# Performance work log

Measured on AMD Instinct MI355X. Metric: run time of the kernel, lower is better.

## Reference

```python
import jax, jax.numpy as jnp
import numpy as np

EPS = 1e-5

def _bn(x, g, b, axes):
    # BatchNorm (training-mode batch statistics), channel axis = 1
    m = jnp.mean(x, axis=axes, keepdims=True)
    v = jnp.var(x, axis=axes, keepdims=True)
    sh = [1] * x.ndim
    sh[1] = -1
    return (x - m) * jax.lax.rsqrt(v + EPS) * g.reshape(sh) + b.reshape(sh)

def _gelu(x):
    return jax.nn.gelu(x, approximate=False)  # torch nn.GELU default (erf)

def _knn_idx(x, k):
    # x: (B, C, N). Negative squared pairwise distance, take k nearest.
    inner = jnp.einsum('bcn,bcm->bnm', x, x)
    sq = jnp.sum(x * x, axis=1)                       # (B, N)
    negd = 2.0 * inner - sq[:, :, None] - sq[:, None, :]
    _, idx = jax.lax.top_k(negd, k)                   # (B, N, k) int32
    return idx

def _graph_feature(x, k):
    # x: (B, C, N) -> (B, 2C, N, k): concat(neighbor - center, center)
    idx = _knn_idx(x, k)
    xt = jnp.transpose(x, (0, 2, 1))                  # (B, N, C)
    nbr = jax.vmap(lambda xb, ib: xb[ib])(xt, idx)    # (B, N, k, C) gather
    ctr = jnp.broadcast_to(xt[:, :, None, :], nbr.shape)
    f = jnp.concatenate([nbr - ctr, ctr], axis=-1)    # (B, N, k, 2C)
    return jnp.transpose(f, (0, 3, 1, 2))             # (B, 2C, N, k)

def _edge_block(x, W, g, b, k):
    # gather -> 1x1 conv -> BN -> GELU -> max over neighbors
    f = _graph_feature(x, k)
    h = jnp.einsum('oi,bink->bonk', W, f)
    h = _gelu(_bn(h, g, b, (0, 2, 3)))
    return jnp.max(h, axis=-1)                        # (B, O, N)


def setup_inputs() -> dict:
    key = jax.random.key(0)
    ks = jax.random.split(key, 16)
    B, C, N, k = 8, 3, 1024, 20
    c = 64
    def w(kk, o, i):
        return jax.random.normal(kk, (o, i), jnp.float32) * (1.0 / np.sqrt(i))
    inp = {
        'x': jax.random.normal(ks[0], (B, C, N), jnp.float32),
        'k': k,
        'W1': w(ks[1], c, 2 * C),            # (64, 6)
        'g1': jnp.ones((c,)), 'b1': jnp.zeros((c,)),
        'W2': w(ks[2], 2 * c, 2 * c),        # (128, 128)
        'g2': jnp.ones((2 * c,)), 'b2': jnp.zeros((2 * c,)),
        'W3': w(ks[3], 4 * c, 4 * c),        # (256, 256)
        'g3': jnp.ones((4 * c,)), 'b3': jnp.zeros((4 * c,)),
        'W4': w(ks[4], 8 * c, 8 * c),        # (512, 512)
        'g4': jnp.ones((8 * c,)), 'b4': jnp.zeros((8 * c,)),
        'W5': w(ks[5], 16 * c, 15 * c),      # (1024, 960) cat(64+128+256+512)
        'g5': jnp.ones((16 * c,)), 'b5': jnp.zeros((16 * c,)),
        'Wl1': w(ks[6], 8 * c, 32 * c),      # (512, 2048), bias=False
        'g6': jnp.ones((8 * c,)), 'b6': jnp.zeros((8 * c,)),
        'Wl2': w(ks[7], 256, 512), 'bl2': jnp.zeros((256,)),
        'g7': jnp.ones((256,)), 'b7': jnp.zeros((256,)),
        'Wl3': w(ks[8], 40, 256), 'bl3': jnp.zeros((40,)),
    }
    return inp


def reference(x, k, W1, g1, b1, W2, g2, b2, W3, g3, b3, W4, g4, b4,
              W5, g5, b5, Wl1, g6, b6, Wl2, bl2, g7, b7, Wl3, bl3):
    x1 = _edge_block(x,  W1, g1, b1, k)   # (B, 64,  N)
    x2 = _edge_block(x1, W2, g2, b2, k)   # (B, 128, N)
    x3 = _edge_block(x2, W3, g3, b3, k)   # (B, 256, N)
    x4 = _edge_block(x3, W4, g4, b4, k)   # (B, 512, N)
    xc = jnp.concatenate([x1, x2, x3, x4], axis=1)  # (B, 960, N)
    h = jnp.einsum('oi,bin->bon', W5, xc)           # (B, 1024, N)
    h = _gelu(_bn(h, g5, b5, (0, 2)))
    mx = jnp.max(h, axis=-1)
    av = jnp.mean(h, axis=-1)
    z = jnp.concatenate([mx, av], axis=1)           # (B, 2048)
    z = z @ Wl1.T                                   # (B, 512), no bias
    z = jax.nn.leaky_relu(_bn(z, g6, b6, (0,)), 0.2)
    z = z @ Wl2.T + bl2                             # (B, 256)
    z = jax.nn.leaky_relu(_bn(z, g7, b7, (0,)), 0.2)
    out = z @ Wl3.T + bl3                           # (B, 40)
    return out
```

## Files before the change

kernel.cpp:

```cpp
#include <hip/hip_runtime.h>
#include <math.h>

#define BB 8
#define NN 1024
#define KNN 20

typedef unsigned short u16;
typedef __bf16 bf16x8 __attribute__((ext_vector_type(8)));
typedef float floatx4 __attribute__((ext_vector_type(4)));

__device__ __forceinline__ float gelu_erf(float x) {
    return 0.5f * x * (1.0f + erff(x * 0.70710678118654752440f));
}

__device__ __forceinline__ u16 f2bf(float f) {
    unsigned int u = __float_as_uint(f);
    unsigned int r = (u + 0x7fffu + ((u >> 16) & 1u)) >> 16;
    return (u16)r;
}
__device__ __forceinline__ float bf2f(u16 h) {
    return __uint_as_float(((unsigned int)h) << 16);
}

#define STATS_BLK 32768
#define STATS_TOTAL (4 * STATS_BLK + 16384)
#define ZERO_TOTAL (STATS_TOTAL + 3 * 8192)

__global__ void k_transpose(const float* __restrict__ x, float* __restrict__ x0,
                            float* __restrict__ sz) {
    int t = blockIdx.x * 256 + threadIdx.x;
    for (int i = t; i < ZERO_TOTAL; i += BB * NN) sz[i] = 0.f;
    if (t >= BB * NN) return;
    int b = t / NN, n = t % NN;
    #pragma unroll
    for (int c = 0; c < 3; ++c) x0[(size_t)t * 3 + c] = x[((size_t)b * 3 + c) * NN + n];
}

#define SEG2 16384
#define SEG3 81920
#define SEG4 344064
#define SEGT 1327104
__global__ void k_prep_w(const float* __restrict__ W2, const float* __restrict__ W3,
                         const float* __restrict__ W4, const float* __restrict__ W5,
                         u16* __restrict__ wh, u16* __restrict__ wl) {
    int t = blockIdx.x * 256 + threadIdx.x;
    if (t >= SEGT) return;
    float v;
    if (t < SEG2) {
        int row = t >> 6, c = t & 63;
        v = (row < 128) ? W2[row * 128 + c]
                        : W2[(row - 128) * 128 + 64 + c] - W2[(row - 128) * 128 + c];
    } else if (t < SEG3) {
        int i = t - SEG2;
        int row = i >> 7, c = i & 127;
        v = (row < 256) ? W3[row * 256 + c]
                        : W3[(row - 256) * 256 + 128 + c] - W3[(row - 256) * 256 + c];
    } else if (t < SEG4) {
        int i = t - SEG3;
        int row = i >> 8, c = i & 255;
        v = (row < 512) ? W4[row * 512 + c]
                        : W4[(row - 512) * 512 + 256 + c] - W4[(row - 512) * 512 + c];
    } else {
        int i = t - SEG4;
        int row = i / 960, c = i % 960;
        v = W5[row * 960 + c];
    }
    u16 h = f2bf(v);
    wh[t] = h;
    wl[t] = f2bf(v - bf2f(h));
}

__global__ void k_negd(const float* __restrict__ X, int SA, int Kc, float* __restrict__ out) {
    int bz = blockIdx.z;
    const float* Xb = X + (size_t)bz * NN * SA;
    float* Cout = out + (size_t)bz * NN * NN;
    int m0 = blockIdx.y * 128, n0 = blockIdx.x * 128;
    __shared__ float As[16][132];
    __shared__ float Bs[16][132];
    __shared__ float sqA[128];
    __shared__ float sqB[128];
    int t = threadIdx.x;
    int tx = t & 15, ty = t >> 4;
    int r = t >> 1, kb = (t & 1) * 8;
    float acc[2][2][4][4] = {};
    float sqa = 0.f, sqb = 0.f;
    for (int k0 = 0; k0 < Kc; k0 += 16) {
        const float* srcA = Xb + (size_t)(m0 + r) * SA + k0 + kb;
        const float* srcB = Xb + (size_t)(n0 + r) * SA + k0 + kb;
        #pragma unroll
        for (int i = 0; i < 8; ++i) {
            float va = (k0 + kb + i < Kc) ? srcA[i] : 0.f;
            float vb = (k0 + kb + i < Kc) ? srcB[i] : 0.f;
            As[kb + i][r] = va;
            Bs[kb + i][r] = vb;
            sqa = fmaf(va, va, sqa);
            sqb = fmaf(vb, vb, sqb);
        }
        __syncthreads();
        #pragma unroll
        for (int kk = 0; kk < 16; ++kk) {
            float4 a0 = *(const float4*)&As[kk][ty * 4];
            float4 a1 = *(const float4*)&As[kk][64 + ty * 4];
            float4 b0 = *(const float4*)&Bs[kk][tx * 4];
            float4 b1 = *(const float4*)&Bs[kk][64 + tx * 4];
            float av[2][4] = {{a0.x, a0.y, a0.z, a0.w}, {a1.x, a1.y, a1.z, a1.w}};
            float bv[2][4] = {{b0.x, b0.y, b0.z, b0.w}, {b1.x, b1.y, b1.z, b1.w}};
            #pragma unroll
            for (int hm = 0; hm < 2; ++hm)
                #pragma unroll
                for (int hn = 0; hn < 2; ++hn)
                    #pragma unroll
                    for (int i = 0; i < 4; ++i)
                        #pragma unroll
                        for (int j = 0; j < 4; ++j)
                            acc[hm][hn][i][j] = fmaf(av[hm][i], bv[hn][j], acc[hm][hn][i][j]);
        }
        __syncthreads();
    }
    sqa += __shfl_xor(sqa, 1);
    sqb += __shfl_xor(sqb, 1);
    if ((t & 1) == 0) { sqA[r] = sqa; sqB[r] = sqb; }
    __syncthreads();
    #pragma unroll
    for (int hm = 0; hm < 2; ++hm)
        #pragma unroll
        for (int i = 0; i < 4; ++i) {
            int lrow = hm * 64 + ty * 4 + i;
            float sm = sqA[lrow];
            float* crow = Cout + (size_t)(m0 + lrow) * NN + n0;
            #pragma unroll
            for (int hn = 0; hn < 2; ++hn) {
                float4 sn = *(const float4*)&sqB[hn * 64 + tx * 4];
                float4 v;
                v.x = 2.f * acc[hm][hn][i][0] - sm - sn.x;
                v.y = 2.f * acc[hm][hn][i][1] - sm - sn.y;
                v.z = 2.f * acc[hm][hn][i][2] - sm - sn.z;
                v.w = 2.f * acc[hm][hn][i][3] - sm - sn.w;
                *(float4*)&crow[hn * 64 + tx * 4] = v;
            }
        }
}

__global__ __launch_bounds__(256) void k_mfma_comb(
    const u16* __restrict__ Ah, const u16* __restrict__ Al,
    const u16* __restrict__ Wh, const u16* __restrict__ Wl,
    const float* __restrict__ sqg,
    float* __restrict__ negdOut, float* __restrict__ uwOut,
    int K, int ldUw) {
    const int lda = 960;
    int bx = blockIdx.x, by = blockIdx.y;
    bool gram = (by < 8);
    int m0, n0, rowBase;
    const u16 *pBh, *pBl;
    size_t ldb;
    float* pC;
    if (gram) {
        int b = bx & 7;
        n0 = (bx >> 3) * 128;
        m0 = by * 128;
        rowBase = b * NN;
        pBh = Ah; pBl = Al; ldb = lda;
        pC = negdOut + (size_t)b * NN * NN;
    } else {
        m0 = bx * 128;
        n0 = (by - 8) * 128;
        rowBase = 0;
        pBh = Wh; pBl = Wl; ldb = K;
        pC = uwOut;
    }
    __shared__ u16 sAh[128 * 40];
    __shared__ u16 sAl[128 * 40];
    __shared__ u16 sBh[128 * 40];
    __shared__ u16 sBl[128 * 40];
    __shared__ float sqA[128];
    __shared__ float sqB[128];
    int t = threadIdx.x;
    int w = t >> 6, lane = t & 63;
    int wm = (w & 1) * 64, wn = (w >> 1) * 64;
    int q = lane >> 4, lm = lane & 15;
    int r = t >> 1, cb = (t & 1) * 16;
    if (gram) {
        if (t < 128) sqA[t] = sqg[rowBase + m0 + t];
        else if (t < 256) sqB[t - 128] = sqg[rowBase + n0 + (t - 128)];
    }
    floatx4 acc[4][4];
    #pragma unroll
    for (int i = 0; i < 4; ++i)
        #pragma unroll
        for (int j = 0; j < 4; ++j) {
            floatx4 z = {0.f, 0.f, 0.f, 0.f};
            acc[i][j] = z;
        }
    for (int k0 = 0; k0 < K; k0 += 32) {
        {
            size_t oa = (size_t)(rowBase + m0 + r) * lda + k0 + cb;
            size_t ob = gram ? (size_t)(rowBase + n0 + r) * lda + k0 + cb
                             : (size_t)(n0 + r) * ldb + k0 + cb;
            float4 ah0 = *(const float4*)&Ah[oa];
            float4 ah1 = *(const float4*)&Ah[oa + 8];
            float4 al0 = *(const float4*)&Al[oa];
            float4 al1 = *(const float4*)&Al[oa + 8];
            float4 bh0 = *(const float4*)&pBh[ob];
            float4 bh1 = *(const float4*)&pBh[ob + 8];
            float4 bl0 = *(const float4*)&pBl[ob];
            float4 bl1 = *(const float4*)&pBl[ob + 8];
            *(float4*)&sAh[r * 40 + cb] = ah0;
            *(float4*)&sAh[r * 40 + cb + 8] = ah1;
            *(float4*)&sAl[r * 40 + cb] = al0;
            *(float4*)&sAl[r * 40 + cb + 8] = al1;
            *(float4*)&sBh[r * 40 + cb] = bh0;
            *(float4*)&sBh[r * 40 + cb + 8] = bh1;
            *(float4*)&sBl[r * 40 + cb] = bl0;
            *(float4*)&sBl[r * 40 + cb + 8] = bl1;
        }
        __syncthreads();
        bf16x8 ah[4], al[4], bh[4], bl[4];
        #pragma unroll
        for (int i = 0; i < 4; ++i) {
            ah[i] = *(const bf16x8*)&sAh[(wm + i * 16 + lm) * 40 + q * 8];
            al[i] = *(const bf16x8*)&sAl[(wm + i * 16 + lm) * 40 + q * 8];
        }
        #pragma unroll
        for (int j = 0; j < 4; ++j) {
            bh[j] = *(const bf16x8*)&sBh[(wn + j * 16 + lm) * 40 + q * 8];
            bl[j] = *(const bf16x8*)&sBl[(wn + j * 16 + lm) * 40 + q * 8];
        }
        #pragma unroll
        for (int i = 0; i < 4; ++i)
            #pragma unroll
            for (int j = 0; j < 4; ++j) {
                acc[i][j] = __builtin_amdgcn_mfma_f32_16x16x32_bf16(ah[i], bh[j], acc[i][j], 0, 0, 0);
                acc[i][j] = __builtin_amdgcn_mfma_f32_16x16x32_bf16(ah[i], bl[j], acc[i][j], 0, 0, 0);
                acc[i][j] = __builtin_amdgcn_mfma_f32_16x16x32_bf16(al[i], bh[j], acc[i][j], 0, 0, 0);
            }
        __syncthreads();
    }
    if (gram) {
        #pragma unroll
        for (int i = 0; i < 4; ++i)
            #pragma unroll
            for (int j = 0; j < 4; ++j) {
                int coll = wn + j * 16 + lm;
                float sn = sqB[coll];
                #pragma unroll
                for (int rr = 0; rr < 4; ++rr) {
                    int rowl = wm + i * 16 + q * 4 + rr;
                    pC[(size_t)(m0 + rowl) * NN + n0 + coll] =
                        2.f * acc[i][j][rr] - sqA[rowl] - sn;
                }
            }
    } else {
        #pragma unroll
        for (int i = 0; i < 4; ++i) {
            int rowb = m0 + wm + i * 16 + q * 4;
            #pragma unroll
            for (int j = 0; j < 4; ++j) {
                int col = n0 + wn + j * 16 + lm;
                #pragma unroll
                for (int rr = 0; rr < 4; ++rr)
                    pC[(size_t)(rowb + rr) * ldUw + col] = acc[i][j][rr];
            }
        }
    }
}

__global__ __launch_bounds__(256) void k_mfma16(
    const u16* __restrict__ Ah, const u16* __restrict__ Al, int lda,
    const u16* __restrict__ Bh, const u16* __restrict__ Bl, int ldb,
    float* __restrict__ Cout, int ldc, int K) {
    int m0 = blockIdx.y * 128, n0 = blockIdx.x * 128;
    __shared__ u16 sAh[128 * 40];
    __shared__ u16 sAl[128 * 40];
    __shared__ u16 sBh[128 * 40];
    __shared__ u16 sBl[128 * 40];
    int t = threadIdx.x;
    int w = t >> 6, lane = t & 63;
    int wm = (w & 1) * 64, wn = (w >> 1) * 64;
    int q = lane >> 4, lm = lane & 15;
    int r = t >> 1, cb = (t & 1) * 16;
    floatx4 acc[4][4];
    #pragma unroll
    for (int i = 0; i < 4; ++i)
        #pragma unroll
        for (int j = 0; j < 4; ++j) {
            floatx4 z = {0.f, 0.f, 0.f, 0.f};
            acc[i][j] = z;
        }
    for (int k0 = 0; k0 < K; k0 += 32) {
        {
            size_t oa = (size_t)(m0 + r) * lda + k0 + cb;
            size_t ob = (size_t)(n0 + r) * ldb + k0 + cb;
            float4 ah0 = *(const float4*)&Ah[oa];
            float4 ah1 = *(const float4*)&Ah[oa + 8];
            float4 al0 = *(const float4*)&Al[oa];
            float4 al1 = *(const float4*)&Al[oa + 8];
            float4 bh0 = *(const float4*)&Bh[ob];
            float4 bh1 = *(const float4*)&Bh[ob + 8];
            float4 bl0 = *(const float4*)&Bl[ob];
            float4 bl1 = *(const float4*)&Bl[ob + 8];
            *(float4*)&sAh[r * 40 + cb] = ah0;
            *(float4*)&sAh[r * 40 + cb + 8] = ah1;
            *(float4*)&sAl[r * 40 + cb] = al0;
            *(float4*)&sAl[r * 40 + cb + 8] = al1;
            *(float4*)&sBh[r * 40 + cb] = bh0;
            *(float4*)&sBh[r * 40 + cb + 8] = bh1;
            *(float4*)&sBl[r * 40 + cb] = bl0;
            *(float4*)&sBl[r * 40 + cb + 8] = bl1;
        }
        __syncthreads();
        bf16x8 ah[4], al[4], bh[4], bl[4];
        #pragma unroll
        for (int i = 0; i < 4; ++i) {
            ah[i] = *(const bf16x8*)&sAh[(wm + i * 16 + lm) * 40 + q * 8];
            al[i] = *(const bf16x8*)&sAl[(wm + i * 16 + lm) * 40 + q * 8];
        }
        #pragma unroll
        for (int j = 0; j < 4; ++j) {
            bh[j] = *(const bf16x8*)&sBh[(wn + j * 16 + lm) * 40 + q * 8];
            bl[j] = *(const bf16x8*)&sBl[(wn + j * 16 + lm) * 40 + q * 8];
        }
        #pragma unroll
        for (int i = 0; i < 4; ++i)
            #pragma unroll
            for (int j = 0; j < 4; ++j) {
                acc[i][j] = __builtin_amdgcn_mfma_f32_16x16x32_bf16(ah[i], bh[j], acc[i][j], 0, 0, 0);
                acc[i][j] = __builtin_amdgcn_mfma_f32_16x16x32_bf16(ah[i], bl[j], acc[i][j], 0, 0, 0);
                acc[i][j] = __builtin_amdgcn_mfma_f32_16x16x32_bf16(al[i], bh[j], acc[i][j], 0, 0, 0);
            }
        __syncthreads();
    }
    #pragma unroll
    for (int i = 0; i < 4; ++i) {
        int rowb = m0 + wm + i * 16 + q * 4;
        #pragma unroll
        for (int j = 0; j < 4; ++j) {
            int col = n0 + wn + j * 16 + lm;
            #pragma unroll
            for (int rr = 0; rr < 4; ++rr)
                Cout[(size_t)(rowb + rr) * ldc + col] = acc[i][j][rr];
        }
    }
}

__global__ void k_topk(const float* __restrict__ negd, int* __restrict__ idxout) {
    int wv = threadIdx.x >> 6, lane = threadIdx.x & 63;
    int rowA = blockIdx.x * 8 + wv * 2;
    int rowB = rowA + 1;
    const float* dA = negd + (size_t)rowA * NN;
    const float* dB = negd + (size_t)rowB * NN;
    float va[16], vb[16];
    #pragma unroll
    for (int j = 0; j < 16; ++j) {
        va[j] = dA[j * 64 + lane];
        vb[j] = dB[j * 64 + lane];
    }
    float lva = va[0], lvb = vb[0];
    int lca = lane, lcb = lane;
    #pragma unroll
    for (int j = 1; j < 16; ++j) {
        int c = j * 64 + lane;
        if (va[j] > lva) { lva = va[j]; lca = c; }
        if (vb[j] > lvb) { lvb = vb[j]; lcb = c; }
    }
    for (int it = 0; it < KNN; ++it) {
        float ta = lva, tb = lvb;
        #pragma unroll
        for (int s = 32; s >= 1; s >>= 1) {
            float oa = __shfl_xor(ta, s);
            float ob = __shfl_xor(tb, s);
            ta = fmaxf(ta, oa);
            tb = fmaxf(tb, ob);
        }
        unsigned long long ma = __ballot(lva == ta);
        unsigned long long mb = __ballot(lvb == tb);
        int wa = 0x7fffffff, wb = 0x7fffffff;
        while (ma) {
            int l = __ffsll((unsigned long long)ma) - 1;
            int c = __shfl(lca, l);
            wa = min(wa, c);
            ma &= ma - 1;
        }
        while (mb) {
            int l = __ffsll((unsigned long long)mb) - 1;
            int c = __shfl(lcb, l);
            wb = min(wb, c);
            mb &= mb - 1;
        }
        if (lane == 0) {
            idxout[(size_t)rowA * KNN + it] = wa;
            idxout[(size_t)rowB * KNN + it] = wb;
        }
        if ((wa & 63) == lane) {
            int jd = wa >> 6;
            #pragma unroll
            for (int j = 0; j < 16; ++j)
                if (j == jd) va[j] = -INFINITY;
            lva = -INFINITY; lca = 0x7fffffff;
            #pragma unroll
            for (int j = 0; j < 16; ++j) {
                int c = j * 64 + lane;
                if (va[j] > lva) { lva = va[j]; lca = c; }
            }
        }
        if ((wb & 63) == lane) {
            int jd = wb >> 6;
            #pragma unroll
            for (int j = 0; j < 16; ++j)
                if (j == jd) vb[j] = -INFINITY;
            lvb = -INFINITY; lcb = 0x7fffffff;
            #pragma unroll
            for (int j = 0; j < 16; ++j) {
                int c = j * 64 + lane;
                if (vb[j] > lvb) { lvb = vb[j]; lcb = c; }
            }
        }
    }
}

__global__ void k_uw1(const float* __restrict__ x0, const float* __restrict__ W1,
                      float* __restrict__ uw) {
    int t = blockIdx.x * 256 + threadIdx.x;
    if (t >= BB * NN * 128) return;
    int r = t >> 7, o = t & 127;
    float xv0 = x0[(size_t)r * 3], xv1 = x0[(size_t)r * 3 + 1], xv2 = x0[(size_t)r * 3 + 2];
    float acc;
    if (o < 64) {
        const float* wr = W1 + (size_t)o * 6;
        acc = wr[0] * xv0 + wr[1] * xv1 + wr[2] * xv2;
    } else {
        const float* wr = W1 + (size_t)(o - 64) * 6;
        acc = (wr[3] - wr[0]) * xv0 + (wr[4] - wr[1]) * xv1 + (wr[5] - wr[2]) * xv2;
    }
    uw[(size_t)t] = acc;
}

__global__ void k_gather4(const float* __restrict__ uw, const int* __restrict__ idx,
                          int O, int ctc, int R,
                          float* __restrict__ hmin, float* __restrict__ hmax,
                          float* __restrict__ s1, float* __restrict__ s2) {
    int t = threadIdx.x;
    int ct = t % ctc, rt = t / ctc;
    int rowsPer = (R * ctc) >> 8;
    int bx = blockIdx.x;
    int b = bx & 7, rg = bx >> 3;
    int row0 = b * NN + rg * R;
    int shard = bx & 15;
    int o4 = blockIdx.y * (ctc * 4) + ct * 4;
    __shared__ int sidx[16 * KNN];
    __shared__ float4 red1[256];
    __shared__ float4 red2[256];
    for (int i = t; i < R * KNN; i += 256) sidx[i] = idx[(size_t)row0 * KNN + i];
    __syncthreads();
    int twoO = 2 * O;
    const float* ubase = uw + (size_t)b * NN * twoO;
    float a1[4] = {0, 0, 0, 0}, a2[4] = {0, 0, 0, 0};
    for (int rr = rt * rowsPer; rr < (rt + 1) * rowsPer; ++rr) {
        int nrow = row0 + rr;
        float4 w4 = *(const float4*)(uw + (size_t)nrow * twoO + O + o4);
        float wv[4] = {w4.x, w4.y, w4.z, w4.w};
        float mn[4], mx[4];
        #pragma unroll
        for (int qq = 0; qq < 4; ++qq) { mn[qq] = INFINITY; mx[qq] = -INFINITY; }
        #pragma unroll 4
        for (int j = 0; j < KNN; ++j) {
            int m = sidx[rr * KNN + j];
            float4 u4 = *(const float4*)(ubase + (size_t)m * twoO + o4);
            float uv[4] = {u4.x, u4.y, u4.z, u4.w};
            #pragma unroll
            for (int qq = 0; qq < 4; ++qq) {
                float h = uv[qq] + wv[qq];
                mn[qq] = fminf(mn[qq], h);
                mx[qq] = fmaxf(mx[qq], h);
                a1[qq] += h;
                a2[qq] = fmaf(h, h, a2[qq]);
            }
        }
        *(float4*)&hmin[(size_t)nrow * O + o4] = make_float4(mn[0], mn[1], mn[2], mn[3]);
        *(float4*)&hmax[(size_t)nrow * O + o4] = make_float4(mx[0], mx[1], mx[2], mx[3]);
    }
    red1[t] = make_float4(a1[0], a1[1], a1[2], a1[3]);
    red2[t] = make_float4(a2[0], a2[1], a2[2], a2[3]);
    __syncthreads();
    if (rt == 0) {
        int rs = 256 / ctc;
        for (int rr = 1; rr < rs; ++rr) {
            float4 v1 = red1[ct + rr * ctc];
            float4 v2 = red2[ct + rr * ctc];
            a1[0] += v1.x; a1[1] += v1.y; a1[2] += v1.z; a1[3] += v1.w;
            a2[0] += v2.x; a2[1] += v2.y; a2[2] += v2.z; a2[3] += v2.w;
        }
        #pragma unroll
        for (int qq = 0; qq < 4; ++qq) {
            atomicAdd(&s1[shard * O + o4 + qq], a1[qq]);
            atomicAdd(&s2[shard * O + o4 + qq], a2[qq]);
        }
    }
}

__global__ void k_bnfin(const float* __restrict__ s1, const float* __restrict__ s2,
                        const float* __restrict__ g, const float* __restrict__ b,
                        float cnt_inv, int O, float* __restrict__ scale,
                        float* __restrict__ shift) {
    int o = blockIdx.x * 256 + threadIdx.x;
    if (o >= O) return;
    float a1 = 0.f, a2 = 0.f;
    #pragma unroll
    for (int s = 0; s < 16; ++s) {
        a1 += s1[s * O + o];
        a2 += s2[s * O + o];
    }
    float mean = a1 * cnt_inv;
    float var = a2 * cnt_inv - mean * mean;
    float sc = g[o] * rsqrtf(var + 1e-5f);
    scale[o] = sc;
    shift[o] = b[o] - mean * sc;
}

__global__ void k_apply(const float* __restrict__ hmin, const float* __restrict__ hmax,
                        const float* __restrict__ scale, const float* __restrict__ shiftv,
                        int O, int shift,
                        u16* __restrict__ outh, u16* __restrict__ outl, int coloff,
                        float* __restrict__ sqout) {
    int gidx = blockIdx.x * 256 + threadIdx.x;
    int row = gidx >> shift;
    int o4 = (gidx & ((1 << shift) - 1)) * 4;
    ushort4 vh, vl;
    float sq = 0.f;
    float vals[4];
    #pragma unroll
    for (int qq = 0; qq < 4; ++qq) {
        int o = o4 + qq;
        float sc = scale[o], sh = shiftv[o];
        float va = gelu_erf(fmaf(sc, hmax[(size_t)row * O + o], sh));
        float vb = gelu_erf(fmaf(sc, hmin[(size_t)row * O + o], sh));
        vals[qq] = fmaxf(va, vb);
        sq = fmaf(vals[qq], vals[qq], sq);
    }
    vh.x = f2bf(vals[0]); vl.x = f2bf(vals[0] - bf2f(vh.x));
    vh.y = f2bf(vals[1]); vl.y = f2bf(vals[1] - bf2f(vh.y));
    vh.z = f2bf(vals[2]); vl.z = f2bf(vals[2] - bf2f(vh.z));
    vh.w = f2bf(vals[3]); vl.w = f2bf(vals[3] - bf2f(vh.w));
    *(ushort4*)&outh[(size_t)row * 960 + coloff + o4] = vh;
    *(ushort4*)&outl[(size_t)row * 960 + coloff + o4] = vl;
    if (sqout) {
        int gsz = 1 << shift;
        if (gsz > 64) gsz = 64;
        #pragma unroll
        for (int s = 1; s < 64; s <<= 1) {
            if (s < gsz) sq += __shfl_xor(sq, s);
        }
        if ((threadIdx.x & (gsz - 1)) == 0) atomicAdd(&sqout[row], sq);
    }
}

__global__ void k_colstats(const float* __restrict__ A, float* __restrict__ s1,
                           float* __restrict__ s2) {
    int o = blockIdx.x * 256 + threadIdx.x;
    int r0 = blockIdx.y * 64;
    int shard = blockIdx.y & 7;
    float a1 = 0.f, a2 = 0.f;
    for (int r = 0; r < 64; ++r) {
        float v = A[(size_t)(r0 + r) * 1024 + o];
        a1 += v;
        a2 = fmaf(v, v, a2);
    }
    atomicAdd(&s1[shard * 1024 + o], a1);
    atomicAdd(&s2[shard * 1024 + o], a2);
}

__global__ void k_apply5(const float* __restrict__ h5, const float* __restrict__ s1,
                         const float* __restrict__ s2, const float* __restrict__ g,
                         const float* __restrict__ b, float* __restrict__ pmax,
                         float* __restrict__ psum) {
    int o = blockIdx.x * 256 + threadIdx.x;
    int ch = blockIdx.y;
    int bb = blockIdx.z;
    float a1 = 0.f, a2 = 0.f;
    #pragma unroll
    for (int s = 0; s < 8; ++s) {
        a1 += s1[s * 1024 + o];
        a2 += s2[s * 1024 + o];
    }
    float mean = a1 * (1.0f / (BB * NN));
    float var = a2 * (1.0f / (BB * NN)) - mean * mean;
    float sc = g[o] * rsqrtf(var + 1e-5f);
    float sh = b[o] - mean * sc;
    int n0 = ch * (NN / 16);
    float mx = -INFINITY, sm = 0.f;
    for (int n = n0; n < n0 + NN / 16; ++n) {
        float v = gelu_erf(fmaf(sc, h5[((size_t)bb * NN + n) * 1024 + o], sh));
        mx = fmaxf(mx, v);
        sm += v;
    }
    pmax[((size_t)ch * BB + bb) * 1024 + o] = mx;
    psum[((size_t)ch * BB + bb) * 1024 + o] = sm;
}

__global__ void k_zfin(const float* __restrict__ pmax, const float* __restrict__ psum,
                       float* __restrict__ z) {
    int o = blockIdx.x * 256 + threadIdx.x;
    int bb = blockIdx.y;
    float mx = -INFINITY, sm = 0.f;
    for (int ch = 0; ch < 16; ++ch) {
        mx = fmaxf(mx, pmax[((size_t)ch * BB + bb) * 1024 + o]);
        sm += psum[((size_t)ch * BB + bb) * 1024 + o];
    }
    z[(size_t)bb * 2048 + o] = mx;
    z[(size_t)bb * 2048 + 1024 + o] = sm * (1.0f / NN);
}

template <int DOBN>
__global__ void k_fc(const float* __restrict__ Z, int Kc, const float* __restrict__ W,
                     const float* __restrict__ bias, const float* __restrict__ g,
                     const float* __restrict__ b, float* __restrict__ out, int Oc) {
    int o = blockIdx.x;
    int lane = threadIdx.x;
    float acc[BB];
    #pragma unroll
    for (int q = 0; q < BB; ++q) acc[q] = 0.f;
    const float* wrow = W + (size_t)o * Kc;
    for (int i = lane; i < Kc; i += 64) {
        float wv = wrow[i];
        #pragma unroll
        for (int q = 0; q < BB; ++q) acc[q] = fmaf(Z[(size_t)q * Kc + i], wv, acc[q]);
    }
    #pragma unroll
    for (int s = 32; s > 0; s >>= 1) {
        #pragma unroll
        for (int q = 0; q < BB; ++q) acc[q] += __shfl_xor(acc[q], s);
    }
    if (lane == 0) {
        float bv = bias ? bias[o] : 0.f;
        float v[BB];
        #pragma unroll
        for (int q = 0; q < BB; ++q) v[q] = acc[q] + bv;
        if (DOBN) {
            float m = 0.f;
            #pragma unroll
            for (int q = 0; q < BB; ++q) m += v[q];
            m *= (1.0f / BB);
            float var = 0.f;
            #pragma unroll
            for (int q = 0; q < BB; ++q) { float d = v[q] - m; var = fmaf(d, d, var); }
            var *= (1.0f / BB);
            float sc = g[o] * rsqrtf(var + 1e-5f);
            #pragma unroll
            for (int q = 0; q < BB; ++q) {
                float y = fmaf(v[q] - m, sc, b[o]);
                v[q] = (y >= 0.f) ? y : 0.2f * y;
            }
        }
        #pragma unroll
        for (int q = 0; q < BB; ++q) out[(size_t)q * Oc + o] = v[q];
    }
}

extern "C" void kernel_launch(void* const* d_in, const int* in_sizes, int n_in,
                              void* d_out, int out_size, void* d_ws, size_t ws_size,
                              hipStream_t stream) {
    (void)in_sizes; (void)n_in; (void)out_size; (void)ws_size;
    const float* x   = (const float*)d_in[0];
    const float* W1  = (const float*)d_in[2];
    const float* g1  = (const float*)d_in[3];
    const float* b1  = (const float*)d_in[4];
    const float* W2  = (const float*)d_in[5];
    const float* g2  = (const float*)d_in[6];
    const float* b2  = (const float*)d_in[7];
    const float* W3  = (const float*)d_in[8];
    const float* g3  = (const float*)d_in[9];
    const float* b3  = (const float*)d_in[10];
    const float* W4  = (const float*)d_in[11];
    const float* g4  = (const float*)d_in[12];
    const float* b4  = (const float*)d_in[13];
    const float* W5  = (const float*)d_in[14];
    const float* g5  = (const float*)d_in[15];
    const float* b5  = (const float*)d_in[16];
    const float* Wl1 = (const float*)d_in[17];
    const float* g6  = (const float*)d_in[18];
    const float* b6  = (const float*)d_in[19];
    const float* Wl2 = (const float*)d_in[20];
    const float* bl2 = (const float*)d_in[21];
    const float* g7  = (const float*)d_in[22];
    const float* b7  = (const float*)d_in[23];
    const float* Wl3 = (const float*)d_in[24];
    const float* bl3 = (const float*)d_in[25];

    char* p = (char*)d_ws;
    auto carve = [&](size_t nbytes) {
        char* q = p;
        p += (nbytes + 255) & ~(size_t)255;
        return (void*)q;
    };
    float* x0   = (float*)carve((size_t)BB * NN * 3 * 4);
    float* negd = (float*)carve((size_t)BB * NN * NN * 4);
    int*   idx  = (int*)carve((size_t)BB * NN * KNN * 4);
    float* uw   = (float*)carve((size_t)BB * NN * 1024 * 4);
    u16*   xch  = (u16*)carve((size_t)BB * NN * 960 * 2);
    u16*   xcl  = (u16*)carve((size_t)BB * NN * 960 * 2);
    u16*   wh   = (u16*)carve((size_t)SEGT * 2);
    u16*   wl   = (u16*)carve((size_t)SEGT * 2);
    float* sz   = (float*)carve((size_t)ZERO_TOTAL * 4);
    float* sqb  = sz + STATS_TOTAL;
    float* scale= (float*)carve(1024 * 4);
    float* shiftv = (float*)carve(1024 * 4);
    float* pmax = (float*)carve((size_t)16 * BB * 1024 * 4);
    float* psum = (float*)carve((size_t)16 * BB * 1024 * 4);
    float* z    = (float*)carve((size_t)BB * 2048 * 4);
    float* z1   = (float*)carve((size_t)BB * 512 * 4);
    float* z2   = (float*)carve((size_t)BB * 256 * 4);
    float* hmin = negd;
    float* hmax = negd + (size_t)BB * NN * 512;

    k_transpose<<<dim3(32), dim3(256), 0, stream>>>(x, x0, sz);
    k_prep_w<<<dim3(SEGT / 256), dim3(256), 0, stream>>>(W2, W3, W4, W5, wh, wl);

    const float* gs[4] = {g1, g2, g3, g4};
    const float* bs[4] = {b1, b2, b3, b4};
    int Cs[4] = {3, 64, 128, 256};
    int Os[4] = {64, 128, 256, 512};
    int coloff[4] = {0, 64, 192, 448};
    int ioff[4]   = {0, 0, 64, 192};
    int woff[4] = {0, 0, SEG2, SEG3};
    int ctcs[4] = {16, 32, 64, 64};
    int gys[4]  = {1, 1, 1, 2};
    int Rs[4]   = {16, 8, 8, 8};
    int shifts[4] = {4, 5, 6, 7};
    float cnt_inv = 1.0f / ((float)BB * NN * KNN);

    for (int blk = 0; blk < 4; ++blk) {
        int C = Cs[blk], O = Os[blk];
        if (blk == 0) {
            k_negd<<<dim3(8, 8, BB), dim3(256), 0, stream>>>(x0, 3, 3, negd);
            k_topk<<<dim3(BB * NN / 8), dim3(256), 0, stream>>>(negd, idx);
            k_uw1<<<dim3(BB * NN * 128 / 256), dim3(256), 0, stream>>>(x0, W1, uw);
        } else {
            k_mfma_comb<<<dim3(64, 8 + 2 * O / 128), dim3(256), 0, stream>>>(
                xch + ioff[blk], xcl + ioff[blk],
                wh + woff[blk], wl + woff[blk],
                sqb + (blk - 1) * 8192, negd, uw, C, 2 * O);
            k_topk<<<dim3(BB * NN / 8), dim3(256), 0, stream>>>(negd, idx);
        }
        float* s1 = sz + blk * STATS_BLK;
        float* s2 = s1 + 16 * O;
        k_gather4<<<dim3(8 * (NN / Rs[blk]), gys[blk]), dim3(256), 0, stream>>>(
            uw, idx, O, ctcs[blk], Rs[blk], hmin, hmax, s1, s2);
        k_bnfin<<<dim3((O + 255) / 256), dim3(256), 0, stream>>>(
            s1, s2, gs[blk], bs[blk], cnt_inv, O, scale, shiftv);
        k_apply<<<dim3(BB * NN * (O / 4) / 256), dim3(256), 0, stream>>>(
            hmin, hmax, scale, shiftv, O, shifts[blk],
            xch, xcl, coloff[blk], (blk < 3) ? (sqb + blk * 8192) : (float*)nullptr);
    }

    k_mfma16<<<dim3(8, 64), dim3(256), 0, stream>>>(
        xch, xcl, 960, wh + SEG4, wl + SEG4, 960, uw, 1024, 960);
    float* s15 = sz + 4 * STATS_BLK;
    float* s25 = s15 + 8 * 1024;
    k_colstats<<<dim3(4, BB * NN / 64), dim3(256), 0, stream>>>(uw, s15, s25);
    k_apply5<<<dim3(4, 16, BB), dim3(256), 0, stream>>>(uw, s15, s25, g5, b5, pmax, psum);
    k_zfin<<<dim3(4, BB), dim3(256), 0, stream>>>(pmax, psum, z);

    k_fc<1><<<dim3(512), dim3(64), 0, stream>>>(z, 2048, Wl1, (const float*)nullptr, g6, b6, z1, 512);
    k_fc<1><<<dim3(256), dim3(64), 0, stream>>>(z1, 512, Wl2, bl2, g7, b7, z2, 256);
    k_fc<0><<<dim3(40), dim3(64), 0, stream>>>(z2, 256, Wl3, bl3, (const float*)nullptr,
                                               (const float*)nullptr, (float*)d_out, 40);
}
```

Baseline: 622.7 us.

## Use k-chunk-major LDS layout in MFMA GEMMs; batch four rows per wave in top-k

After: 681.8 us. 1.09x slower.

```diff
diff --git a/kernel.cpp b/kernel.cpp
--- a/kernel.cpp
+++ b/kernel.cpp
@@ -168,10 +168,10 @@
         pBh = Wh; pBl = Wl; ldb = K;
         pC = uwOut;
     }
-    __shared__ u16 sAh[128 * 40];
-    __shared__ u16 sAl[128 * 40];
-    __shared__ u16 sBh[128 * 40];
-    __shared__ u16 sBl[128 * 40];
+    __shared__ u16 sAh[4 * 1024];
+    __shared__ u16 sAl[4 * 1024];
+    __shared__ u16 sBh[4 * 1024];
+    __shared__ u16 sBl[4 * 1024];
     __shared__ float sqA[128];
     __shared__ float sqB[128];
     int t = threadIdx.x;
@@ -179,6 +179,7 @@
     int wm = (w & 1) * 64, wn = (w >> 1) * 64;
     int q = lane >> 4, lm = lane & 15;
     int r = t >> 1, cb = (t & 1) * 16;
+    int q0 = (t & 1) * 2;
     if (gram) {
         if (t < 128) sqA[t] = sqg[rowBase + m0 + t];
         else if (t < 256) sqB[t - 128] = sqg[rowBase + n0 + (t - 128)];
@@ -204,26 +205,26 @@
             float4 bh1 = *(const float4*)&pBh[ob + 8];
             float4 bl0 = *(const float4*)&pBl[ob];
             float4 bl1 = *(const float4*)&pBl[ob + 8];
-            *(float4*)&sAh[r * 40 + cb] = ah0;
-            *(float4*)&sAh[r * 40 + cb + 8] = ah1;
-            *(float4*)&sAl[r * 40 + cb] = al0;
-            *(float4*)&sAl[r * 40 + cb + 8] = al1;
-            *(float4*)&sBh[r * 40 + cb] = bh0;
-            *(float4*)&sBh[r * 40 + cb + 8] = bh1;
-            *(float4*)&sBl[r * 40 + cb] = bl0;
-            *(float4*)&sBl[r * 40 + cb + 8] = bl1;
+            *(float4*)&sAh[q0 * 1024 + r * 8] = ah0;
+            *(float4*)&sAh[(q0 + 1) * 1024 + r * 8] = ah1;
+            *(float4*)&sAl[q0 * 1024 + r * 8] = al0;
+            *(float4*)&sAl[(q0 + 1) * 1024 + r * 8] = al1;
+            *(float4*)&sBh[q0 * 1024 + r * 8] = bh0;
+            *(float4*)&sBh[(q0 + 1) * 1024 + r * 8] = bh1;
+            *(float4*)&sBl[q0 * 1024 + r * 8] = bl0;
+            *(float4*)&sBl[(q0 + 1) * 1024 + r * 8] = bl1;
         }
         __syncthreads();
         bf16x8 ah[4], al[4], bh[4], bl[4];
         #pragma unroll
         for (int i = 0; i < 4; ++i) {
-            ah[i] = *(const bf16x8*)&sAh[(wm + i * 16 + lm) * 40 + q * 8];
-            al[i] = *(const bf16x8*)&sAl[(wm + i * 16 + lm) * 40 + q * 8];
+            ah[i] = *(const bf16x8*)&sAh[q * 1024 + (wm + i * 16 + lm) * 8];
+            al[i] = *(const bf16x8*)&sAl[q * 1024 + (wm + i * 16 + lm) * 8];
         }
         #pragma unroll
         for (int j = 0; j < 4; ++j) {
-            bh[j] = *(const bf16x8*)&sBh[(wn + j * 16 + lm) * 40 + q * 8];
-            bl[j] = *(const bf16x8*)&sBl[(wn + j * 16 + lm) * 40 + q * 8];
+            bh[j] = *(const bf16x8*)&sBh[q * 1024 + (wn + j * 16 + lm) * 8];
+            bl[j] = *(const bf16x8*)&sBl[q * 1024 + (wn + j * 16 + lm) * 8];
         }
         #pragma unroll
         for (int i = 0; i < 4; ++i)
@@ -269,15 +270,16 @@
     const u16* __restrict__ Bh, const u16* __restrict__ Bl, int ldb,
     float* __restrict__ Cout, int ldc, int K) {
     int m0 = blockIdx.y * 128, n0 = blockIdx.x * 128;
-    __shared__ u16 sAh[128 * 40];
-    __shared__ u16 sAl[128 * 40];
-    __shared__ u16 sBh[128 * 40];
-    __shared__ u16 sBl[128 * 40];
+    __shared__ u16 sAh[4 * 1024];
+    __shared__ u16 sAl[4 * 1024];
+    __shared__ u16 sBh[4 * 1024];
+    __shared__ u16 sBl[4 * 1024];
     int t = threadIdx.x;
     int w = t >> 6, lane = t & 63;
     int wm = (w & 1) * 64, wn = (w >> 1) * 64;
     int q = lane >> 4, lm = lane & 15;
     int r = t >> 1, cb = (t & 1) * 16;
+    int q0 = (t & 1) * 2;
     floatx4 acc[4][4];
     #pragma unroll
     for (int i = 0; i < 4; ++i)
@@ -298,26 +300,26 @@
             float4 bh1 = *(const float4*)&Bh[ob + 8];
             float4 bl0 = *(const float4*)&Bl[ob];
             float4 bl1 = *(const float4*)&Bl[ob + 8];
-            *(float4*)&sAh[r * 40 + cb] = ah0;
-            *(float4*)&sAh[r * 40 + cb + 8] = ah1;
-            *(float4*)&sAl[r * 40 + cb] = al0;
-            *(float4*)&sAl[r * 40 + cb + 8] = al1;
-            *(float4*)&sBh[r * 40 + cb] = bh0;
-            *(float4*)&sBh[r * 40 + cb + 8] = bh1;
-            *(float4*)&sBl[r * 40 + cb] = bl0;
-            *(float4*)&sBl[r * 40 + cb + 8] = bl1;
+            *(float4*)&sAh[q0 * 1024 + r * 8] = ah0;
+            *(float4*)&sAh[(q0 + 1) * 1024 + r * 8] = ah1;
+            *(float4*)&sAl[q0 * 1024 + r * 8] = al0;
+            *(float4*)&sAl[(q0 + 1) * 1024 + r * 8] = al1;
+            *(float4*)&sBh[q0 * 1024 + r * 8] = bh0;
+            *(float4*)&sBh[(q0 + 1) * 1024 + r * 8] = bh1;
+            *(float4*)&sBl[q0 * 1024 + r * 8] = bl0;
+            *(float4*)&sBl[(q0 + 1) * 1024 + r * 8] = bl1;
         }
         __syncthreads();
         bf16x8 ah[4], al[4], bh[4], bl[4];
         #pragma unroll
         for (int i = 0; i < 4; ++i) {
-            ah[i] = *(const bf16x8*)&sAh[(wm + i * 16 + lm) * 40 + q * 8];
-            al[i] = *(const bf16x8*)&sAl[(wm + i * 16 + lm) * 40 + q * 8];
+            ah[i] = *(const bf16x8*)&sAh[q * 1024 + (wm + i * 16 + lm) * 8];
+            al[i] = *(const bf16x8*)&sAl[q * 1024 + (wm + i * 16 + lm) * 8];
         }
         #pragma unroll
         for (int j = 0; j < 4; ++j) {
-            bh[j] = *(const bf16x8*)&sBh[(wn + j * 16 + lm) * 40 + q * 8];
-            bl[j] = *(const bf16x8*)&sBl[(wn + j * 16 + lm) * 40 + q * 8];
+            bh[j] = *(const bf16x8*)&sBh[q * 1024 + (wn + j * 16 + lm) * 8];
+            bl[j] = *(const bf16x8*)&sBl[q * 1024 + (wn + j * 16 + lm) * 8];
         }
         #pragma unroll
         for (int i = 0; i < 4; ++i)
@@ -344,74 +346,60 @@
 
 __global__ void k_topk(const float* __restrict__ negd, int* __restrict__ idxout) {
     int wv = threadIdx.x >> 6, lane = threadIdx.x & 63;
-    int rowA = blockIdx.x * 8 + wv * 2;
-    int rowB = rowA + 1;
-    const float* dA = negd + (size_t)rowA * NN;
-    const float* dB = negd + (size_t)rowB * NN;
-    float va[16], vb[16];
-    #pragma unroll
-    for (int j = 0; j < 16; ++j) {
-        va[j] = dA[j * 64 + lane];
-        vb[j] = dB[j * 64 + lane];
-    }
-    float lva = va[0], lvb = vb[0];
-    int lca = lane, lcb = lane;
-    #pragma unroll
-    for (int j = 1; j < 16; ++j) {
-        int c = j * 64 + lane;
-        if (va[j] > lva) { lva = va[j]; lca = c; }
-        if (vb[j] > lvb) { lvb = vb[j]; lcb = c; }
+    int row0 = blockIdx.x * 16 + wv * 4;
+    unsigned v[4][16];
+    #pragma unroll
+    for (int rr = 0; rr < 4; ++rr) {
+        const float* d = negd + (size_t)(row0 + rr) * NN;
+        #pragma unroll
+        for (int j = 0; j < 16; ++j) {
+            unsigned u = __float_as_uint(d[j * 64 + lane]);
+            v[rr][j] = u ^ ((unsigned)((int)u >> 31) | 0x80000000u);
+        }
+    }
+    unsigned lv[4];
+    int lc[4];
+    #pragma unroll
+    for (int rr = 0; rr < 4; ++rr) {
+        lv[rr] = v[rr][0];
+        lc[rr] = lane;
+        #pragma unroll
+        for (int j = 1; j < 16; ++j)
+            if (v[rr][j] > lv[rr]) { lv[rr] = v[rr][j]; lc[rr] = j * 64 + lane; }
     }
     for (int it = 0; it < KNN; ++it) {
-        float ta = lva, tb = lvb;
+        unsigned tv[4];
+        #pragma unroll
+        for (int rr = 0; rr < 4; ++rr) tv[rr] = lv[rr];
         #pragma unroll
         for (int s = 32; s >= 1; s >>= 1) {
-            float oa = __shfl_xor(ta, s);
-            float ob = __shfl_xor(tb, s);
-            ta = fmaxf(ta, oa);
-            tb = fmaxf(tb, ob);
-        }
-        unsigned long long ma = __ballot(lva == ta);
-        unsigned long long mb = __ballot(lvb == tb);
-        int wa = 0x7fffffff, wb = 0x7fffffff;
-        while (ma) {
-            int l = __ffsll((unsigned long long)ma) - 1;
-            int c = __shfl(lca, l);
-            wa = min(wa, c);
-            ma &= ma - 1;
-        }
-        while (mb) {
-            int l = __ffsll((unsigned long long)mb) - 1;
-            int c = __shfl(lcb, l);
-            wb = min(wb, c);
-            mb &= mb - 1;
-        }
-        if (lane == 0) {
-            idxout[(size_t)rowA * KNN + it] = wa;
-            idxout[(size_t)rowB * KNN + it] = wb;
-        }
-        if ((wa & 63) == lane) {
-            int jd = wa >> 6;
-            #pragma unroll
-            for (int j = 0; j < 16; ++j)
-                if (j == jd) va[j] = -INFINITY;
-            lva = -INFINITY; lca = 0x7fffffff;
-            #pragma unroll
-            for (int j = 0; j < 16; ++j) {
-                int c = j * 64 + lane;
-                if (va[j] > lva) { lva = va[j]; lca = c; }
-            }
-        }
-        if ((wb & 63) == lane) {
-            int jd = wb >> 6;
-            #pragma unroll
-            for (int j = 0; j < 16; ++j)
-                if (j == jd) vb[j] = -INFINITY;
-            lvb = -INFINITY; lcb = 0x7fffffff;
-            #pragma unroll
-            for (int j = 0; j < 16; ++j) {
-                int c = j * 64 + lane;
-                if (vb[j] > lvb) { lvb = vb[j]; lcb = c; }
+            #pragma unroll
+            for (int rr = 0; rr < 4; ++rr) {
+                unsigned o = (unsigned)__shfl_xor((int)tv[rr], s);
+                tv[rr] = (o > tv[rr]) ? o : tv[rr];
+            }
+        }
+        #pragma unroll
+        for (int rr = 0; rr < 4; ++rr) {
+            unsigned long long m = __ballot(lv[rr] == tv[rr]);
+            int win = 0x7fffffff;
+            while (m) {
+                int l = __ffsll(m) - 1;
+                int c = __shfl(lc[rr], l);
+                win = min(win, c);
+                m &= m - 1;
+            }
+            if (lane == 0) idxout[(size_t)(row0 + rr) * KNN + it] = win;
+            if ((win & 63) == lane) {
+                int jd = win >> 6;
+                #pragma unroll
+                for (int j = 0; j < 16; ++j)
+                    if (j == jd) v[rr][j] = 0u;
+                lv[rr] = 0u;
+                lc[rr] = 0x7fffffff;
+                #pragma unroll
+                for (int j = 0; j < 16; ++j)
+                    if (v[rr][j] > lv[rr]) { lv[rr] = v[rr][j]; lc[rr] = j * 64 + lane; }
             }
         }
     }
@@ -731,14 +719,14 @@
         int C = Cs[blk], O = Os[blk];
         if (blk == 0) {
             k_negd<<<dim3(8, 8, BB), dim3(256), 0, stream>>>(x0, 3, 3, negd);
-            k_topk<<<dim3(BB * NN / 8), dim3(256), 0, stream>>>(negd, idx);
+            k_topk<<<dim3(BB * NN / 16), dim3(256), 0, stream>>>(negd, idx);
             k_uw1<<<dim3(BB * NN * 128 / 256), dim3(256), 0, stream>>>(x0, W1, uw);
         } else {
             k_mfma_comb<<<dim3(64, 8 + 2 * O / 128), dim3(256), 0, stream>>>(
                 xch + ioff[blk], xcl + ioff[blk],
                 wh + woff[blk], wl + woff[blk],
                 sqb + (blk - 1) * 8192, negd, uw, C, 2 * O);
-            k_topk<<<dim3(BB * NN / 8), dim3(256), 0, stream>>>(negd, idx);
+            k_topk<<<dim3(BB * NN / 16), dim3(256), 0, stream>>>(negd, idx);
         }
         float* s1 = sz + blk * STATS_BLK;
         float* s2 = s1 + 16 * O;
```
